# Performance work log

Hardware: AMD Instinct MI355X
Metric: run time of the kernel (lower is better)

The kernel has to match this reference:

```python
import jax, jax.numpy as jnp
import numpy as np

NUM_HEADS = 12
EPS = 1e-4


def setup_inputs() -> dict:
    key = jax.random.key(0)
    k1, k2, k3 = jax.random.split(key, 3)
    C = 768
    B, N = 128, 196  # B = b * num_frames = 8 * 16
    x = jax.random.normal(k1, (B, N, C), dtype=jnp.float32)
    W_qkv = jax.random.normal(k2, (3 * C, C), dtype=jnp.float32) * 0.02
    W_proj = jax.random.normal(k3, (C, C), dtype=jnp.float32) * 0.02
    b_proj = jnp.zeros((C,), dtype=jnp.float32)
    return {"x": x, "W_qkv": W_qkv, "W_proj": W_proj, "b_proj": b_proj,
            "num_frames": 16}


def reference(x, W_qkv, W_proj, b_proj, num_frames):
    B, N, C = x.shape
    h = NUM_HEADS
    e = C // h
    # qkv projection (no bias), split k-first then heads: 'b n (k h e)'
    qkv = (x @ W_qkv.T).reshape(B, N, 3, h, e)
    q, k, v = qkv[:, :, 0], qkv[:, :, 1], qkv[:, :, 2]  # [B, N, h, e]
    q_ = jax.nn.relu(q)
    k_ = jax.nn.relu(k)
    # fold frames into the sequence: (b f) n -> b (f n)
    b = B // num_frames
    S = num_frames * N
    q_ = q_.reshape(b, S, h, e)
    k_ = k_.reshape(b, S, h, e)
    v_ = v.reshape(b, S, h, e)
    # kv trick: kv[b,h,e,d] = sum_s k[b,s,h,e] v[b,s,h,d]
    kv = jnp.einsum('bshe,bshd->bhed', k_, v_)
    k_sum = k_.sum(axis=1)  # [b, h, e]
    z = 1.0 / (jnp.einsum('bshe,bhe->bsh', q_, k_sum) + EPS)  # [b, S, h]
    out = jnp.einsum('bshe,bhed->bshd', q_, kv) * z[..., None]  # [b, S, h, e]
    out = out.reshape(B, N, C)
    # output projection (dropouts are identity at eval)
    return out @ W_proj.T + b_proj
```

## Files before the change

kernel.cpp:

```cpp
#include <hip/hip_runtime.h>
#include <hip/hip_bf16.h>

#define EPS_Z 1e-4f

typedef __attribute__((ext_vector_type(8))) short bf16x8;
typedef __attribute__((ext_vector_type(4))) float f32x4;

__device__ __forceinline__ float b2f(short s) {
    union { unsigned u; float f; } cv;
    cv.u = ((unsigned)(unsigned short)s) << 16;
    return cv.f;
}

__device__ __forceinline__ void gld_lds16(const __hip_bfloat16* g, __hip_bfloat16* l) {
    __builtin_amdgcn_global_load_lds(
        (__attribute__((address_space(1))) void*)(g),
        (__attribute__((address_space(3))) void*)(l),
        16, 0, 0);
}

__global__ __launch_bounds__(256)
void cvt_f32_bf16(const float* __restrict__ in, __hip_bfloat16* __restrict__ out, int n4)
{
    int i = blockIdx.x * 256 + threadIdx.x;
    if (i >= n4) return;
    float4 v = ((const float4*)in)[i];
    union { short4 s; __hip_bfloat16 h[4]; } o;
    o.h[0] = __float2bfloat16(v.x);
    o.h[1] = __float2bfloat16(v.y);
    o.h[2] = __float2bfloat16(v.z);
    o.h[3] = __float2bfloat16(v.w);
    ((short4*)out)[i] = o.s;
}

template<int MODE, typename CT>
__global__ __launch_bounds__(256, 2)
void gemm_bt(const __hip_bfloat16* __restrict__ A,
             const __hip_bfloat16* __restrict__ B,
             CT* __restrict__ C,
             const float* __restrict__ bias,
             int K, int N, int gx)
{
    __shared__ __align__(16) __hip_bfloat16 As[128 * 64];
    __shared__ __align__(16) __hip_bfloat16 Bs[128 * 64];
    const int g = blockIdx.x;
    const int gp = (g & 7) * ((int)gridDim.x >> 3) + (g >> 3);
    const int bx = gp % gx;
    const int by = gp / gx;

    const int tid = threadIdx.x;
    const int w = tid >> 6;
    const int l = tid & 63;
    const int wr = (w >> 1) * 64;
    const int wc = (w & 1) * 64;
    const int l15 = l & 15;
    const int lq = l >> 4;
    const int rx = l15 & 7;

    f32x4 acc[4][4] = {};

    const int srow8 = l >> 3;
    const int scol = (((l & 7) ^ (l >> 3)) << 3);

    const __hip_bfloat16* Ab = A + (size_t)by * 128 * K;
    const __hip_bfloat16* Bb = B + (size_t)bx * 128 * K;

    for (int k0 = 0; k0 < K; k0 += 64) {
        __syncthreads();
        #pragma unroll
        for (int i = 0; i < 4; ++i) {
            const int chunk = w * 4 + i;
            const int row = chunk * 8 + srow8;
            gld_lds16(Ab + (size_t)row * K + (k0 + scol), As + chunk * 512);
            gld_lds16(Bb + (size_t)row * K + (k0 + scol), Bs + chunk * 512);
        }
        __syncthreads();
        #pragma unroll
        for (int kk = 0; kk < 64; kk += 32) {
            const int kb = (kk >> 3) + lq;
            const int col = (kb ^ rx) << 3;
            bf16x8 a[4], b[4];
            #pragma unroll
            for (int i = 0; i < 4; ++i)
                a[i] = *(const bf16x8*)(As + (wr + i * 16 + l15) * 64 + col);
            #pragma unroll
            for (int j = 0; j < 4; ++j)
                b[j] = *(const bf16x8*)(Bs + (wc + j * 16 + l15) * 64 + col);
            #pragma unroll
            for (int i = 0; i < 4; ++i)
                #pragma unroll
                for (int j = 0; j < 4; ++j)
                    acc[i][j] = __builtin_amdgcn_mfma_f32_16x16x32_bf16(a[i], b[j], acc[i][j], 0, 0, 0);
        }
    }

    const int crow0 = by * 128 + wr + lq * 4;
    const int ccol0 = bx * 128 + wc + l15;
    #pragma unroll
    for (int i = 0; i < 4; ++i) {
        #pragma unroll
        for (int j = 0; j < 4; ++j) {
            const int gc = ccol0 + j * 16;
            const float badd = (MODE == 2) ? bias[gc] : 0.0f;
            #pragma unroll
            for (int r = 0; r < 4; ++r) {
                const int gr = crow0 + i * 16 + r;
                float v = acc[i][j][r];
                if (MODE == 1 && gc < 1536) v = fmaxf(v, 0.0f);
                if (MODE == 2) v += badd;
                if (MODE == 1)
                    ((__hip_bfloat16*)C)[(size_t)gr * N + gc] = __float2bfloat16(v);
                else
                    ((float*)C)[(size_t)gr * N + gc] = v;
            }
        }
    }
}

__global__ __launch_bounds__(256)
void kv_mfma_kernel(const __hip_bfloat16* __restrict__ qkv,
                    float* __restrict__ kvg, float* __restrict__ ksumg)
{
    const int SPLIT = 14;
    const int bh = blockIdx.x / SPLIT;
    const int ck = blockIdx.x % SPLIT;
    const int b = bh / 12, h = bh % 12;

    __shared__ __align__(16) __hip_bfloat16 kT[64 * 40];
    __shared__ __align__(16) __hip_bfloat16 vT[64 * 40];

    const int tid = threadIdx.x;
    const int w = tid >> 6, l = tid & 63;
    const int l15 = l & 15, lq = l >> 4;

    const int half = tid >> 7;
    const int idx  = tid & 127;
    const int e0 = (idx >> 4) * 8;
    const int sp = idx & 15;

    const size_t rowbase = (size_t)b * 3136 * 2304 + (half ? 1536 : 768) + h * 64 + e0;
    __hip_bfloat16* Tdst = half ? vT : kT;

    f32x4 acc[4] = {};
    f32x4 accks = {};

    bf16x8 ones;
    #pragma unroll
    for (int i = 0; i < 8; ++i) ones[i] = (short)0x3F80;

    const int s_begin = ck * 224;
    for (int s0 = s_begin; s0 < s_begin + 224; s0 += 32) {
        __syncthreads();
        bf16x8 r0 = *(const bf16x8*)(qkv + rowbase + (size_t)(s0 + 2 * sp) * 2304);
        bf16x8 r1 = *(const bf16x8*)(qkv + rowbase + (size_t)(s0 + 2 * sp + 1) * 2304);
        #pragma unroll
        for (int q = 0; q < 8; ++q) {
            unsigned pk = ((unsigned)(unsigned short)r0[q]) |
                          (((unsigned)(unsigned short)r1[q]) << 16);
            *(unsigned*)(Tdst + (e0 + q) * 40 + 2 * sp) = pk;
        }
        __syncthreads();
        bf16x8 a = *(const bf16x8*)(vT + (w * 16 + l15) * 40 + lq * 8);
        bf16x8 bfr[4];
        #pragma unroll
        for (int j = 0; j < 4; ++j)
            bfr[j] = *(const bf16x8*)(kT + (j * 16 + l15) * 40 + lq * 8);
        #pragma unroll
        for (int j = 0; j < 4; ++j)
            acc[j] = __builtin_amdgcn_mfma_f32_16x16x32_bf16(a, bfr[j], acc[j], 0, 0, 0);
        accks = __builtin_amdgcn_mfma_f32_16x16x32_bf16(ones, bfr[w], accks, 0, 0, 0);
    }

    float* kvdst = kvg + ((size_t)bh << 12);
    #pragma unroll
    for (int j = 0; j < 4; ++j) {
        const int col = j * 16 + l15;
        #pragma unroll
        for (int r = 0; r < 4; ++r) {
            const int row = w * 16 + lq * 4 + r;
            atomicAdd(kvdst + row * 64 + col, acc[j][r]);
        }
    }
    if (lq == 0)
        atomicAdd(ksumg + (bh << 6) + w * 16 + l15, accks[0]);
}

__global__ __launch_bounds__(256)
void attn_mfma2(const __hip_bfloat16* __restrict__ qkv,
                const __hip_bfloat16* __restrict__ kvb,
                const float* __restrict__ ksumg,
                __hip_bfloat16* __restrict__ att)
{
    const int bh = blockIdx.x / 49;
    const int mt = blockIdx.x % 49;
    const int b = bh / 12, h = bh % 12;
    const int tid = threadIdx.x;
    const int w = tid >> 6, l = tid & 63;
    const int l15 = l & 15, lq = l >> 4;

    const size_t m0 = (size_t)b * 3136 + (size_t)mt * 64 + w * 16;

    const __hip_bfloat16* qrow = qkv + (m0 + l15) * 2304 + h * 64;
    bf16x8 aq0 = *(const bf16x8*)(qrow + lq * 8);
    bf16x8 aq1 = *(const bf16x8*)(qrow + 32 + lq * 8);

    const float* ks = ksumg + (bh << 6);
    float kse[8], kse1[8];
    *(float4*)(kse)      = *(const float4*)(ks + lq * 8);
    *(float4*)(kse + 4)  = *(const float4*)(ks + lq * 8 + 4);
    *(float4*)(kse1)     = *(const float4*)(ks + 32 + lq * 8);
    *(float4*)(kse1 + 4) = *(const float4*)(ks + 32 + lq * 8 + 4);
    float zp = 0.0f;
    #pragma unroll
    for (int j = 0; j < 8; ++j)
        zp += b2f(aq0[j]) * kse[j] + b2f(aq1[j]) * kse1[j];
    zp += __shfl_xor(zp, 16);
    zp += __shfl_xor(zp, 32);
    const float zr = 1.0f / (zp + EPS_Z);

    const __hip_bfloat16* kvh = kvb + ((size_t)bh << 12);
    f32x4 acc[4] = {};
    #pragma unroll
    for (int j = 0; j < 4; ++j) {
        bf16x8 b0 = *(const bf16x8*)(kvh + (j * 16 + l15) * 64 + lq * 8);
        bf16x8 b1 = *(const bf16x8*)(kvh + (j * 16 + l15) * 64 + 32 + lq * 8);
        acc[j] = __builtin_amdgcn_mfma_f32_16x16x32_bf16(aq0, b0, acc[j], 0, 0, 0);
        acc[j] = __builtin_amdgcn_mfma_f32_16x16x32_bf16(aq1, b1, acc[j], 0, 0, 0);
    }

    float zrow[4];
    #pragma unroll
    for (int r = 0; r < 4; ++r) zrow[r] = __shfl(zr, lq * 4 + r);

    #pragma unroll
    for (int j = 0; j < 4; ++j) {
        const int col = j * 16 + l15;
        #pragma unroll
        for (int r = 0; r < 4; ++r) {
            const int row = lq * 4 + r;
            att[(m0 + row) * 768 + h * 64 + col] = __float2bfloat16(acc[j][r] * zrow[r]);
        }
    }
}

extern "C" void kernel_launch(void* const* d_in, const int* in_sizes, int n_in,
                              void* d_out, int out_size, void* d_ws, size_t ws_size,
                              hipStream_t stream)
{
    const float* x      = (const float*)d_in[0];
    const float* W_qkv  = (const float*)d_in[1];
    const float* W_proj = (const float*)d_in[2];
    const float* b_proj = (const float*)d_in[3];
    float* out = (float*)d_out;

    const int M = 25088, K = 768, N1 = 2304, N2 = 768;

    __hip_bfloat16* qkv = (__hip_bfloat16*)d_ws;
    __hip_bfloat16* xb  = qkv + (size_t)M * N1;
    __hip_bfloat16* wqb = xb + (size_t)M * K;
    __hip_bfloat16* wpb = wqb + (size_t)N1 * K;
    float* kvg  = (float*)(wpb + (size_t)N2 * K);
    float* ksum = kvg + 96 * 4096;
    __hip_bfloat16* kvb = (__hip_bfloat16*)(ksum + 96 * 64);
    __hip_bfloat16* att = xb;

    hipMemsetAsync(kvg, 0, (size_t)(96 * 4096 + 96 * 64) * sizeof(float), stream);

    cvt_f32_bf16<<<(M * K / 4 + 255) / 256, 256, 0, stream>>>(x, xb, M * K / 4);
    cvt_f32_bf16<<<(N1 * K / 4 + 255) / 256, 256, 0, stream>>>(W_qkv, wqb, N1 * K / 4);
    cvt_f32_bf16<<<(N2 * K / 4 + 255) / 256, 256, 0, stream>>>(W_proj, wpb, N2 * K / 4);

    gemm_bt<1, __hip_bfloat16><<<(M / 128) * (N1 / 128), 256, 0, stream>>>(
        xb, wqb, qkv, nullptr, K, N1, N1 / 128);
    kv_mfma_kernel<<<96 * 14, 256, 0, stream>>>(qkv, kvg, ksum);
    cvt_f32_bf16<<<(96 * 4096 / 4 + 255) / 256, 256, 0, stream>>>(kvg, kvb, 96 * 4096 / 4);
    attn_mfma2<<<96 * 49, 256, 0, stream>>>(qkv, kvb, ksum, att);
    gemm_bt<2, float><<<(M / 128) * (N2 / 128), 256, 0, stream>>>(
        att, wpb, out, b_proj, K, N2, N2 / 128);
}
```

Measured before the change: 345.6 us.

## Double-buffer kv reduction loads and process two heads per attention block

The kv reduction kernel now double-buffers its shared-memory transpose tiles and prefetches the next 32-row chunk from global memory into registers while MFMAs run on the current one. This cuts the syncs per iteration from two to one. The attention kernel now handles two adjacent heads per block, so each 16-row Q read covers 128 contiguous bf16 values and half as many blocks are launched. The cost is twice the LDS, more registers for the prefetched rows and second-head accumulators, and less parallelism in the attention launch.

Result: slower. 362.0 us (+4.7%).

```diff
diff --git a/kernel.cpp b/kernel.cpp
--- a/kernel.cpp
+++ b/kernel.cpp
@@ -126,8 +126,8 @@
     const int ck = blockIdx.x % SPLIT;
     const int b = bh / 12, h = bh % 12;
 
-    __shared__ __align__(16) __hip_bfloat16 kT[64 * 40];
-    __shared__ __align__(16) __hip_bfloat16 vT[64 * 40];
+    __shared__ __align__(16) __hip_bfloat16 kT[2][64 * 40];
+    __shared__ __align__(16) __hip_bfloat16 vT[2][64 * 40];
 
     const int tid = threadIdx.x;
     const int w = tid >> 6, l = tid & 63;
@@ -139,7 +139,6 @@
     const int sp = idx & 15;
 
     const size_t rowbase = (size_t)b * 3136 * 2304 + (half ? 1536 : 768) + h * 64 + e0;
-    __hip_bfloat16* Tdst = half ? vT : kT;
 
     f32x4 acc[4] = {};
     f32x4 accks = {};
@@ -149,22 +148,29 @@
     for (int i = 0; i < 8; ++i) ones[i] = (short)0x3F80;
 
     const int s_begin = ck * 224;
-    for (int s0 = s_begin; s0 < s_begin + 224; s0 += 32) {
-        __syncthreads();
-        bf16x8 r0 = *(const bf16x8*)(qkv + rowbase + (size_t)(s0 + 2 * sp) * 2304);
-        bf16x8 r1 = *(const bf16x8*)(qkv + rowbase + (size_t)(s0 + 2 * sp + 1) * 2304);
+    bf16x8 r0 = *(const bf16x8*)(qkv + rowbase + (size_t)(s_begin + 2 * sp) * 2304);
+    bf16x8 r1 = *(const bf16x8*)(qkv + rowbase + (size_t)(s_begin + 2 * sp + 1) * 2304);
+
+    for (int i = 0; i < 7; ++i) {
+        const int buf = i & 1;
+        __hip_bfloat16* Td = half ? vT[buf] : kT[buf];
         #pragma unroll
         for (int q = 0; q < 8; ++q) {
             unsigned pk = ((unsigned)(unsigned short)r0[q]) |
                           (((unsigned)(unsigned short)r1[q]) << 16);
-            *(unsigned*)(Tdst + (e0 + q) * 40 + 2 * sp) = pk;
+            *(unsigned*)(Td + (e0 + q) * 40 + 2 * sp) = pk;
         }
         __syncthreads();
-        bf16x8 a = *(const bf16x8*)(vT + (w * 16 + l15) * 40 + lq * 8);
+        if (i < 6) {
+            const int s0 = s_begin + (i + 1) * 32;
+            r0 = *(const bf16x8*)(qkv + rowbase + (size_t)(s0 + 2 * sp) * 2304);
+            r1 = *(const bf16x8*)(qkv + rowbase + (size_t)(s0 + 2 * sp + 1) * 2304);
+        }
+        bf16x8 a = *(const bf16x8*)(vT[buf] + (w * 16 + l15) * 40 + lq * 8);
         bf16x8 bfr[4];
         #pragma unroll
         for (int j = 0; j < 4; ++j)
-            bfr[j] = *(const bf16x8*)(kT + (j * 16 + l15) * 40 + lq * 8);
+            bfr[j] = *(const bf16x8*)(kT[buf] + (j * 16 + l15) * 40 + lq * 8);
         #pragma unroll
         for (int j = 0; j < 4; ++j)
             acc[j] = __builtin_amdgcn_mfma_f32_16x16x32_bf16(a, bfr[j], acc[j], 0, 0, 0);
@@ -186,59 +192,81 @@
 }
 
 __global__ __launch_bounds__(256)
-void attn_mfma2(const __hip_bfloat16* __restrict__ qkv,
+void attn_mfma3(const __hip_bfloat16* __restrict__ qkv,
                 const __hip_bfloat16* __restrict__ kvb,
                 const float* __restrict__ ksumg,
                 __hip_bfloat16* __restrict__ att)
 {
-    const int bh = blockIdx.x / 49;
-    const int mt = blockIdx.x % 49;
-    const int b = bh / 12, h = bh % 12;
+    const int t = blockIdx.x;
+    const int g = t % 49;
+    const int bhp = t / 49;
+    const int hp = bhp % 6, b = bhp / 6;
     const int tid = threadIdx.x;
     const int w = tid >> 6, l = tid & 63;
     const int l15 = l & 15, lq = l >> 4;
 
-    const size_t m0 = (size_t)b * 3136 + (size_t)mt * 64 + w * 16;
-
-    const __hip_bfloat16* qrow = qkv + (m0 + l15) * 2304 + h * 64;
-    bf16x8 aq0 = *(const bf16x8*)(qrow + lq * 8);
-    bf16x8 aq1 = *(const bf16x8*)(qrow + 32 + lq * 8);
-
-    const float* ks = ksumg + (bh << 6);
-    float kse[8], kse1[8];
-    *(float4*)(kse)      = *(const float4*)(ks + lq * 8);
-    *(float4*)(kse + 4)  = *(const float4*)(ks + lq * 8 + 4);
-    *(float4*)(kse1)     = *(const float4*)(ks + 32 + lq * 8);
-    *(float4*)(kse1 + 4) = *(const float4*)(ks + 32 + lq * 8 + 4);
-    float zp = 0.0f;
-    #pragma unroll
-    for (int j = 0; j < 8; ++j)
-        zp += b2f(aq0[j]) * kse[j] + b2f(aq1[j]) * kse1[j];
-    zp += __shfl_xor(zp, 16);
-    zp += __shfl_xor(zp, 32);
-    const float zr = 1.0f / (zp + EPS_Z);
-
-    const __hip_bfloat16* kvh = kvb + ((size_t)bh << 12);
-    f32x4 acc[4] = {};
-    #pragma unroll
-    for (int j = 0; j < 4; ++j) {
-        bf16x8 b0 = *(const bf16x8*)(kvh + (j * 16 + l15) * 64 + lq * 8);
-        bf16x8 b1 = *(const bf16x8*)(kvh + (j * 16 + l15) * 64 + 32 + lq * 8);
-        acc[j] = __builtin_amdgcn_mfma_f32_16x16x32_bf16(aq0, b0, acc[j], 0, 0, 0);
-        acc[j] = __builtin_amdgcn_mfma_f32_16x16x32_bf16(aq1, b1, acc[j], 0, 0, 0);
-    }
-
-    float zrow[4];
-    #pragma unroll
-    for (int r = 0; r < 4; ++r) zrow[r] = __shfl(zr, lq * 4 + r);
-
-    #pragma unroll
-    for (int j = 0; j < 4; ++j) {
-        const int col = j * 16 + l15;
-        #pragma unroll
-        for (int r = 0; r < 4; ++r) {
-            const int row = lq * 4 + r;
-            att[(m0 + row) * 768 + h * 64 + col] = __float2bfloat16(acc[j][r] * zrow[r]);
+    const int tau = g * 4 + w;
+    const size_t m0 = (size_t)b * 3136 + (size_t)tau * 16;
+    const int h0 = hp * 2;
+    const int bh0 = b * 12 + h0;
+
+    const __hip_bfloat16* qrow = qkv + (m0 + l15) * 2304 + h0 * 64;
+    bf16x8 aq[4];
+    aq[0] = *(const bf16x8*)(qrow + lq * 8);
+    aq[1] = *(const bf16x8*)(qrow + 32 + lq * 8);
+    aq[2] = *(const bf16x8*)(qrow + 64 + lq * 8);
+    aq[3] = *(const bf16x8*)(qrow + 96 + lq * 8);
+
+    const float* ks = ksumg + (bh0 << 6);
+    float kse[4][8];
+    #pragma unroll
+    for (int s = 0; s < 4; ++s) {
+        *(float4*)(kse[s])     = *(const float4*)(ks + s * 32 + lq * 8);
+        *(float4*)(kse[s] + 4) = *(const float4*)(ks + s * 32 + lq * 8 + 4);
+    }
+    float zp0 = 0.0f, zp1 = 0.0f;
+    #pragma unroll
+    for (int j = 0; j < 8; ++j) {
+        zp0 += b2f(aq[0][j]) * kse[0][j] + b2f(aq[1][j]) * kse[1][j];
+        zp1 += b2f(aq[2][j]) * kse[2][j] + b2f(aq[3][j]) * kse[3][j];
+    }
+    zp0 += __shfl_xor(zp0, 16); zp0 += __shfl_xor(zp0, 32);
+    zp1 += __shfl_xor(zp1, 16); zp1 += __shfl_xor(zp1, 32);
+    const float zr0 = 1.0f / (zp0 + EPS_Z);
+    const float zr1 = 1.0f / (zp1 + EPS_Z);
+
+    const __hip_bfloat16* kvh = kvb + ((size_t)bh0 << 12);
+    f32x4 acc[2][4] = {};
+    #pragma unroll
+    for (int hh = 0; hh < 2; ++hh) {
+        #pragma unroll
+        for (int j = 0; j < 4; ++j) {
+            bf16x8 b0 = *(const bf16x8*)(kvh + hh * 4096 + (j * 16 + l15) * 64 + lq * 8);
+            bf16x8 b1 = *(const bf16x8*)(kvh + hh * 4096 + (j * 16 + l15) * 64 + 32 + lq * 8);
+            acc[hh][j] = __builtin_amdgcn_mfma_f32_16x16x32_bf16(aq[hh * 2], b0, acc[hh][j], 0, 0, 0);
+            acc[hh][j] = __builtin_amdgcn_mfma_f32_16x16x32_bf16(aq[hh * 2 + 1], b1, acc[hh][j], 0, 0, 0);
+        }
+    }
+
+    float zrow0[4], zrow1[4];
+    #pragma unroll
+    for (int r = 0; r < 4; ++r) {
+        zrow0[r] = __shfl(zr0, lq * 4 + r);
+        zrow1[r] = __shfl(zr1, lq * 4 + r);
+    }
+
+    #pragma unroll
+    for (int hh = 0; hh < 2; ++hh) {
+        #pragma unroll
+        for (int j = 0; j < 4; ++j) {
+            const int col = j * 16 + l15;
+            #pragma unroll
+            for (int r = 0; r < 4; ++r) {
+                const int row = lq * 4 + r;
+                const float zv = hh ? zrow1[r] : zrow0[r];
+                att[(m0 + row) * 768 + (h0 + hh) * 64 + col] =
+                    __float2bfloat16(acc[hh][j][r] * zv);
+            }
         }
     }
 }
@@ -274,7 +302,7 @@
         xb, wqb, qkv, nullptr, K, N1, N1 / 128);
     kv_mfma_kernel<<<96 * 14, 256, 0, stream>>>(qkv, kvg, ksum);
     cvt_f32_bf16<<<(96 * 4096 / 4 + 255) / 256, 256, 0, stream>>>(kvg, kvb, 96 * 4096 / 4);
-    attn_mfma2<<<96 * 49, 256, 0, stream>>>(qkv, kvb, ksum, att);
+    attn_mfma3<<<96 / 2 * 49, 256, 0, stream>>>(qkv, kvb, ksum, att);
     gemm_bt<2, float><<<(M / 128) * (N2 / 128), 256, 0, stream>>>(
         att, wpb, out, b_proj, K, N2, N2 / 128);
 }
```
